# Performance work log

Hardware: AMD Instinct MI355X
Metric: run time of the kernel (lower is better)

The kernel has to match this reference:

```python
import jax, jax.numpy as jnp
import numpy as np

B, S, D, H = 4, 2048, 1024, 16
DK = D // H

def setup_inputs() -> dict:
    key = jax.random.key(0)
    ks = jax.random.split(key, 11)
    sc = 1.0 / np.sqrt(D)
    return {
        "query": jax.random.normal(ks[0], (B, S, D), jnp.float32),
        "key": jax.random.normal(ks[1], (B, S, D), jnp.float32),
        "value": jax.random.normal(ks[2], (B, S, D), jnp.float32),
        "Wq": jax.random.normal(ks[3], (D, D), jnp.float32) * sc,
        "bq": jnp.zeros((D,), jnp.float32),
        "Wk": jax.random.normal(ks[4], (D, D), jnp.float32) * sc,
        "bk": jnp.zeros((D,), jnp.float32),
        "Wv": jax.random.normal(ks[5], (D, D), jnp.float32) * sc,
        "bv": jnp.zeros((D,), jnp.float32),
        "Wo": jax.random.normal(ks[6], (D, D), jnp.float32) * sc,
        "bo": jnp.zeros((D,), jnp.float32),
    }

def _mha(query, key, value, Wq, bq, Wk, bk, Wv, bv, Wo, bo):
    # in_linear{0,1,2}: y = x @ W.T + b  (MetaLinearLayer, weight [out,in])
    def proj(x, W, b):
        y = jnp.einsum('bsd,ed->bse', x, W) + b
        return y.reshape(B, S, H, DK).transpose(0, 2, 1, 3)  # [B,H,S,DK]
    q = proj(query, Wq, bq)
    k = proj(key, Wk, bk)
    v = proj(value, Wv, bv)
    # scores = QK^T / sqrt(d_k)  -> [B,H,S,S] (materialized as in original)
    scores = jnp.einsum('bhqd,bhkd->bhqk', q, k) / jnp.sqrt(jnp.float32(DK))
    p_attn = jax.nn.softmax(scores, axis=-1)
    # dropout is identity in eval/reference mode
    x = jnp.einsum('bhqk,bhkd->bhqd', p_attn, v)
    x = x.transpose(0, 2, 1, 3).reshape(B, S, D)
    return jnp.einsum('bsd,ed->bse', x, Wo) + bo

def reference(query, key, value, Wq, bq, Wk, bk, Wv, bv, Wo, bo):
    return _mha(query, key, value, Wq, bq, Wk, bk, Wv, bv, Wo, bo)
```

## Files before the change

kernel.cpp:

```cpp
#include <hip/hip_runtime.h>
#include <stdint.h>

typedef __attribute__((ext_vector_type(4))) float f32x4;
typedef __attribute__((ext_vector_type(8))) __bf16 bf16x8;
typedef __attribute__((ext_vector_type(8))) unsigned short u16x8;

#define GLOBAL_AS __attribute__((address_space(1)))
#define LDS_AS    __attribute__((address_space(3)))

__device__ __forceinline__ void lds_load16(const void* g, void* l) {
  __builtin_amdgcn_global_load_lds((const GLOBAL_AS uint32_t*)(uintptr_t)g,
                                   (LDS_AS uint32_t*)(uintptr_t)l, 16, 0, 0);
}

__device__ __forceinline__ unsigned short f2bf(float f) {
  uint32_t u = __builtin_bit_cast(uint32_t, f);
  u += 0x7fffu + ((u >> 16) & 1u);
  return (unsigned short)(u >> 16);
}

__device__ __forceinline__ uint32_t pk_bf16(float a, float b) {
#if __has_builtin(__builtin_amdgcn_cvt_pk_bf16_f32)
  return __builtin_bit_cast(uint32_t, __builtin_amdgcn_cvt_pk_bf16_f32(a, b));
#else
  return (uint32_t)f2bf(a) | ((uint32_t)f2bf(b) << 16);
#endif
}

__global__ void cast_all(const float* __restrict__ q, const float* __restrict__ k,
                         const float* __restrict__ v, const float* __restrict__ Wq,
                         const float* __restrict__ Wk, const float* __restrict__ Wv,
                         const float* __restrict__ Wo, unsigned short* __restrict__ dst) {
  const int bid = blockIdx.x;
  const float* src;
  int rel;
  if (bid < 24576) {
    const int seg = bid >> 13;
    rel = bid & 8191;
    src = (seg == 0) ? q : (seg == 1) ? k : v;
  } else {
    const int w = (bid - 24576) >> 10;
    rel = (bid - 24576) & 1023;
    src = (w == 0) ? Wq : (w == 1) ? Wk : (w == 2) ? Wv : Wo;
  }
  const size_t di = (size_t)bid * 1024 + threadIdx.x * 4;
  const size_t si = (size_t)rel * 1024 + threadIdx.x * 4;
  const float4 val = *(const float4*)(src + si);
  ushort4 o;
  o.x = f2bf(val.x); o.y = f2bf(val.y); o.z = f2bf(val.z); o.w = f2bf(val.w);
  *(ushort4*)(dst + di) = o;
}

__global__ __launch_bounds__(256, 2)
void gemm_qkv(const unsigned short* __restrict__ xq, const unsigned short* __restrict__ xk,
              const unsigned short* __restrict__ xv, const unsigned short* __restrict__ wq,
              const unsigned short* __restrict__ wk, const unsigned short* __restrict__ wv,
              const float* __restrict__ bq, const float* __restrict__ bk,
              const float* __restrict__ bv,
              unsigned short* __restrict__ Qh, unsigned short* __restrict__ Kh,
              unsigned short* __restrict__ Vt)
{
  __shared__ __align__(16) unsigned short As[128 * 32];
  __shared__ __align__(16) unsigned short Bs[128 * 32];

  const int gy = blockIdx.y, gx = blockIdx.x;
  const unsigned short* A  = (gy == 0) ? xq : (gy == 1) ? xk : wv;
  const unsigned short* Bw = (gy == 0) ? wq : (gy == 1) ? wk : xv;
  const float* bias        = (gy == 0) ? bq : (gy == 1) ? bk : bv;

  int m0, n0, N;
  if (gy < 2) { m0 = (gx >> 3) * 128; n0 = (gx & 7) * 128; N = 1024; }
  else        { m0 = (gx & 7) * 128;  n0 = (gx >> 3) * 128; N = 8192; }
  const int K = 1024;

  const int tid  = threadIdx.x;
  const int wave = tid >> 6;
  const int lane = tid & 63;
  const int wm = wave >> 1, wn = wave & 1;
  const int quad = lane >> 4, l15 = lane & 15;

  f32x4 acc[4][4];
#pragma unroll
  for (int i = 0; i < 4; ++i)
#pragma unroll
    for (int j = 0; j < 4; ++j) acc[i][j] = f32x4{0.f, 0.f, 0.f, 0.f};

  const int sr = lane >> 2;
  const int sc = (lane & 3) * 8;
  const unsigned short* Ag0 = A  + (size_t)(m0 + wave * 16 + sr) * K + sc;
  const unsigned short* Ag1 = Ag0 + (size_t)64 * K;
  const unsigned short* Bg0 = Bw + (size_t)(n0 + wave * 16 + sr) * K + sc;
  const unsigned short* Bg1 = Bg0 + (size_t)64 * K;
  unsigned short* AsW0 = &As[wave * 512];
  unsigned short* AsW1 = &As[2048 + wave * 512];
  unsigned short* BsW0 = &Bs[wave * 512];
  unsigned short* BsW1 = &Bs[2048 + wave * 512];

  for (int k0 = 0; k0 < K; k0 += 32) {
    lds_load16(Ag0 + k0, AsW0);
    lds_load16(Ag1 + k0, AsW1);
    lds_load16(Bg0 + k0, BsW0);
    lds_load16(Bg1 + k0, BsW1);
    __syncthreads();

    bf16x8 af[4], bfr[4];
#pragma unroll
    for (int i = 0; i < 4; ++i)
      af[i] = *(const bf16x8*)&As[(wm * 64 + i * 16 + l15) * 32 + quad * 8];
#pragma unroll
    for (int j = 0; j < 4; ++j)
      bfr[j] = *(const bf16x8*)&Bs[(wn * 64 + j * 16 + l15) * 32 + quad * 8];
#pragma unroll
    for (int i = 0; i < 4; ++i)
#pragma unroll
      for (int j = 0; j < 4; ++j)
        acc[i][j] = __builtin_amdgcn_mfma_f32_16x16x32_bf16(af[i], bfr[j], acc[i][j], 0, 0, 0);
    __syncthreads();
  }

  if (gy < 2) {
    unsigned short* out = (gy == 0) ? Qh : Kh;
    float bj[4];
#pragma unroll
    for (int j = 0; j < 4; ++j) bj[j] = bias[n0 + wn * 64 + j * 16 + l15];
#pragma unroll
    for (int i = 0; i < 4; ++i) {
      const int mbase = m0 + wm * 64 + i * 16 + quad * 4;
#pragma unroll
      for (int j = 0; j < 4; ++j) {
        const int n = n0 + wn * 64 + j * 16 + l15;
#pragma unroll
        for (int r = 0; r < 4; ++r) {
          const int m = mbase + r;
          const float vv = acc[i][j][r] + bj[j];
          const size_t idx = ((((size_t)(m >> 11) * 16 + (n >> 6)) << 11) + (size_t)(m & 2047)) * 64 + (n & 63);
          out[idx] = f2bf(vv);
        }
      }
    }
  } else {
#pragma unroll
    for (int i = 0; i < 4; ++i) {
      const int mbase = m0 + wm * 64 + i * 16 + quad * 4;
      float bm[4];
#pragma unroll
      for (int r = 0; r < 4; ++r) bm[r] = bias[mbase + r];
#pragma unroll
      for (int j = 0; j < 4; ++j) {
        const int n = n0 + wn * 64 + j * 16 + l15;
#pragma unroll
        for (int r = 0; r < 4; ++r)
          Vt[(size_t)(mbase + r) * N + n] = f2bf(acc[i][j][r] + bm[r]);
      }
    }
  }
}

__global__ __launch_bounds__(256, 2)
void flash_attn(const unsigned short* __restrict__ Qh,
                const unsigned short* __restrict__ Kh,
                const unsigned short* __restrict__ VtG,
                unsigned short* __restrict__ Xo)
{
  __shared__ __align__(16) unsigned short Ks[128 * 72];
  __shared__ __align__(16) unsigned short Vs[64 * 136];
  __shared__ __align__(16) unsigned short Ps[128 * 136];

  const int qb = blockIdx.x, h = blockIdx.y, b = blockIdx.z;
  const int tid = threadIdx.x, wave = tid >> 6, lane = tid & 63;
  const int quad = lane >> 4, l15 = lane & 15;

  const size_t bh = (((size_t)b * 16 + h) << 17);
  const unsigned short* Qg = Qh + bh + ((size_t)qb << 13);
  const unsigned short* Kg = Kh + bh;
  const unsigned short* Vg = VtG + ((size_t)(h * 64)) * 8192 + (size_t)b * 2048;

#pragma unroll
  for (int p = 0; p < 4; ++p) {
    const int c = tid + p * 256;
    u16x8 qv = *(const u16x8*)(Qg + c * 8);
    *(u16x8*)&Ps[(c >> 3) * 136 + (c & 7) * 8] = qv;
  }
  __syncthreads();
  bf16x8 aq[2][2];
#pragma unroll
  for (int i = 0; i < 2; ++i)
#pragma unroll
    for (int d = 0; d < 2; ++d)
      aq[i][d] = *(const bf16x8*)&Ps[(wave * 32 + i * 16 + l15) * 136 + d * 32 + quad * 8];

  f32x4 oacc[2][4];
  float mrow[2], lrow[2];
#pragma unroll
  for (int i = 0; i < 2; ++i) {
#pragma unroll
    for (int jd = 0; jd < 4; ++jd) oacc[i][jd] = f32x4{0.f, 0.f, 0.f, 0.f};
    mrow[i] = -1e30f; lrow[i] = 0.f;
  }

  u16x8 kreg[4], vreg[4];
#pragma unroll
  for (int p = 0; p < 4; ++p) {
    const int c = tid + p * 256;
    kreg[p] = *(const u16x8*)(Kg + c * 8);
    vreg[p] = *(const u16x8*)(Vg + (size_t)(c >> 4) * 8192 + (c & 15) * 8);
  }

  for (int kb = 0; kb < 16; ++kb) {
    __syncthreads();
#pragma unroll
    for (int p = 0; p < 4; ++p) {
      const int c = tid + p * 256;
      *(u16x8*)&Ks[(c >> 3) * 72 + (c & 7) * 8] = kreg[p];
      *(u16x8*)&Vs[(c >> 4) * 136 + (c & 15) * 8] = vreg[p];
    }
    if (kb < 15) {
      const size_t ko = ((size_t)(kb + 1) << 13);
#pragma unroll
      for (int p = 0; p < 4; ++p) {
        const int c = tid + p * 256;
        kreg[p] = *(const u16x8*)(Kg + ko + c * 8);
        vreg[p] = *(const u16x8*)(Vg + (size_t)(c >> 4) * 8192 + (kb + 1) * 128 + (c & 15) * 8);
      }
    }
    __syncthreads();

    f32x4 s[2][8];
#pragma unroll
    for (int i = 0; i < 2; ++i)
#pragma unroll
      for (int j = 0; j < 8; ++j) s[i][j] = f32x4{0.f, 0.f, 0.f, 0.f};
#pragma unroll
    for (int d = 0; d < 2; ++d)
#pragma unroll
      for (int j = 0; j < 8; ++j) {
        bf16x8 kf = *(const bf16x8*)&Ks[(j * 16 + l15) * 72 + d * 32 + quad * 8];
#pragma unroll
        for (int i = 0; i < 2; ++i)
          s[i][j] = __builtin_amdgcn_mfma_f32_16x16x32_bf16(kf, aq[i][d], s[i][j], 0, 0, 0);
      }

#pragma unroll
    for (int i = 0; i < 2; ++i) {
      float mx = -1e30f;
#pragma unroll
      for (int j = 0; j < 8; ++j)
#pragma unroll
        for (int r = 0; r < 4; ++r) {
          s[i][j][r] *= 0.125f;
          mx = fmaxf(mx, s[i][j][r]);
        }
      mx = fmaxf(mx, __shfl_xor(mx, 16));
      mx = fmaxf(mx, __shfl_xor(mx, 32));
      const float mo = mrow[i];
      const float mn = fmaxf(mo, mx);
      mrow[i] = mn;
      const float al = __expf(mo - mn);
      float rs = 0.f;
#pragma unroll
      for (int j = 0; j < 8; ++j)
#pragma unroll
        for (int r = 0; r < 4; ++r) {
          const float p = __expf(s[i][j][r] - mn);
          s[i][j][r] = p;
          rs += p;
        }
      rs += __shfl_xor(rs, 16);
      rs += __shfl_xor(rs, 32);
      lrow[i] = lrow[i] * al + rs;

#pragma unroll
      for (int r = 0; r < 4; ++r) {
        const float aO = __shfl(al, quad * 4 + r);
#pragma unroll
        for (int jd = 0; jd < 4; ++jd) oacc[i][jd][r] *= aO;
      }

      const int prow = (wave * 32 + i * 16 + l15) * 136;
#pragma unroll
      for (int j = 0; j < 8; ++j) {
        uint2 pk;
        pk.x = pk_bf16(s[i][j][0], s[i][j][1]);
        pk.y = pk_bf16(s[i][j][2], s[i][j][3]);
        *(uint2*)&Ps[prow + j * 16 + quad * 4] = pk;
      }
    }

    asm volatile("" ::: "memory");

#pragma unroll
    for (int kk = 0; kk < 4; ++kk) {
      bf16x8 ap[2];
#pragma unroll
      for (int i = 0; i < 2; ++i)
        ap[i] = *(const bf16x8*)&Ps[(wave * 32 + i * 16 + l15) * 136 + kk * 32 + quad * 8];
#pragma unroll
      for (int jd = 0; jd < 4; ++jd) {
        bf16x8 bv = *(const bf16x8*)&Vs[(jd * 16 + l15) * 136 + kk * 32 + quad * 8];
#pragma unroll
        for (int i = 0; i < 2; ++i)
          oacc[i][jd] = __builtin_amdgcn_mfma_f32_16x16x32_bf16(ap[i], bv, oacc[i][jd], 0, 0, 0);
      }
    }
  }

#pragma unroll
  for (int i = 0; i < 2; ++i)
#pragma unroll
    for (int r = 0; r < 4; ++r) {
      const float lO = __shfl(lrow[i], quad * 4 + r);
      const float inv = 1.f / lO;
      const int srow = qb * 128 + wave * 32 + i * 16 + quad * 4 + r;
      const size_t obase = (((size_t)b << 11) + srow) * 1024 + (h << 6);
#pragma unroll
      for (int jd = 0; jd < 4; ++jd)
        Xo[obase + jd * 16 + l15] = f2bf(oacc[i][jd][r] * inv);
    }
}

__global__ __launch_bounds__(256, 2)
void gemm_out(const unsigned short* __restrict__ A,
              const unsigned short* __restrict__ Bw,
              const float* __restrict__ bias,
              float* __restrict__ Cout)
{
  __shared__ __align__(16) unsigned short As[128 * 32];
  __shared__ __align__(16) unsigned short Bs[128 * 32];

  const int tid  = threadIdx.x;
  const int wave = tid >> 6;
  const int lane = tid & 63;
  const int wm = wave >> 1, wn = wave & 1;
  const int quad = lane >> 4, l15 = lane & 15;
  const int m0 = blockIdx.y * 128;
  const int n0 = blockIdx.x * 128;
  const int K = 1024, N = 1024;

  f32x4 acc[4][4];
#pragma unroll
  for (int i = 0; i < 4; ++i)
#pragma unroll
    for (int j = 0; j < 4; ++j) acc[i][j] = f32x4{0.f, 0.f, 0.f, 0.f};

  const int sr = lane >> 2;
  const int sc = (lane & 3) * 8;
  const unsigned short* Ag0 = A  + (size_t)(m0 + wave * 16 + sr) * K + sc;
  const unsigned short* Ag1 = Ag0 + (size_t)64 * K;
  const unsigned short* Bg0 = Bw + (size_t)(n0 + wave * 16 + sr) * K + sc;
  const unsigned short* Bg1 = Bg0 + (size_t)64 * K;
  unsigned short* AsW0 = &As[wave * 512];
  unsigned short* AsW1 = &As[2048 + wave * 512];
  unsigned short* BsW0 = &Bs[wave * 512];
  unsigned short* BsW1 = &Bs[2048 + wave * 512];

  for (int k0 = 0; k0 < K; k0 += 32) {
    lds_load16(Ag0 + k0, AsW0);
    lds_load16(Ag1 + k0, AsW1);
    lds_load16(Bg0 + k0, BsW0);
    lds_load16(Bg1 + k0, BsW1);
    __syncthreads();

    bf16x8 af[4], bfr[4];
#pragma unroll
    for (int i = 0; i < 4; ++i)
      af[i] = *(const bf16x8*)&As[(wm * 64 + i * 16 + l15) * 32 + quad * 8];
#pragma unroll
    for (int j = 0; j < 4; ++j)
      bfr[j] = *(const bf16x8*)&Bs[(wn * 64 + j * 16 + l15) * 32 + quad * 8];
#pragma unroll
    for (int i = 0; i < 4; ++i)
#pragma unroll
      for (int j = 0; j < 4; ++j)
        acc[i][j] = __builtin_amdgcn_mfma_f32_16x16x32_bf16(af[i], bfr[j], acc[i][j], 0, 0, 0);
    __syncthreads();
  }

  float bj[4];
#pragma unroll
  for (int j = 0; j < 4; ++j) bj[j] = bias[n0 + wn * 64 + j * 16 + l15];

#pragma unroll
  for (int i = 0; i < 4; ++i) {
    const int mbase = m0 + wm * 64 + i * 16 + quad * 4;
#pragma unroll
    for (int j = 0; j < 4; ++j) {
      const int n = n0 + wn * 64 + j * 16 + l15;
#pragma unroll
      for (int r = 0; r < 4; ++r)
        Cout[(size_t)(mbase + r) * N + n] = acc[i][j][r] + bj[j];
    }
  }
}

extern "C" void kernel_launch(void* const* d_in, const int* in_sizes, int n_in,
                              void* d_out, int out_size, void* d_ws, size_t ws_size,
                              hipStream_t stream) {
  const float* q  = (const float*)d_in[0];
  const float* k  = (const float*)d_in[1];
  const float* v  = (const float*)d_in[2];
  const float* Wq = (const float*)d_in[3];
  const float* bq = (const float*)d_in[4];
  const float* Wk = (const float*)d_in[5];
  const float* bk = (const float*)d_in[6];
  const float* Wv = (const float*)d_in[7];
  const float* bv = (const float*)d_in[8];
  const float* Wo = (const float*)d_in[9];
  const float* bo = (const float*)d_in[10];

  const int B = 4, S = 2048, D = 1024, H = 16;
  const size_t NX = (size_t)B * S * D;
  const size_t NW = (size_t)D * D;

  unsigned short* xq = (unsigned short*)d_ws;
  unsigned short* xk = xq + NX;
  unsigned short* xv = xk + NX;
  unsigned short* wq = xv + NX;
  unsigned short* wk = wq + NW;
  unsigned short* wv = wk + NW;
  unsigned short* wo = wv + NW;
  unsigned short* Qh = wo + NW;
  unsigned short* Kh = Qh + NX;
  unsigned short* Vt = Kh + NX;
  unsigned short* xo = Vt + NX;

  cast_all<<<28672, 256, 0, stream>>>(q, k, v, Wq, Wk, Wv, Wo, xq);

  gemm_qkv<<<dim3(512, 3), 256, 0, stream>>>(xq, xk, xv, wq, wk, wv, bq, bk, bv, Qh, Kh, Vt);

  flash_attn<<<dim3(S / 128, H, B), 256, 0, stream>>>(Qh, Kh, Vt, xo);

  gemm_out<<<dim3(D / 128, (B * S) / 128), 256, 0, stream>>>(xo, wo, bo, (float*)d_out);
}
```

Measured before the change: 399.6 us.

## Keep softmax probabilities in registers via permuted K rows, drop P LDS buffer

Flash attention now permutes the K rows as they are stored to LDS, so the QK^T MFMA output lanes line up with the A-operand layout the PV MFMA expects. The probabilities are packed straight from registers into bf16 fragments, which removes the P shared-memory buffer and its write/read round trip. With less LDS in use, launch bounds go from 2 to 4 blocks per CU. The softmax also switches to exp2 with log2(e) folded into the scale factor. The risks are extra register pressure under the tighter launch bound and getting the lane permutation wrong.

```diff
diff --git a/kernel.cpp b/kernel.cpp
--- a/kernel.cpp
+++ b/kernel.cpp
@@ -4,6 +4,7 @@
 typedef __attribute__((ext_vector_type(4))) float f32x4;
 typedef __attribute__((ext_vector_type(8))) __bf16 bf16x8;
 typedef __attribute__((ext_vector_type(8))) unsigned short u16x8;
+typedef __attribute__((ext_vector_type(4))) uint32_t u32x4;
 
 #define GLOBAL_AS __attribute__((address_space(1)))
 #define LDS_AS    __attribute__((address_space(3)))
@@ -25,6 +26,23 @@
 #else
   return (uint32_t)f2bf(a) | ((uint32_t)f2bf(b) << 16);
 #endif
+}
+
+__device__ __forceinline__ float exp2f_fast(float x) {
+#if __has_builtin(__builtin_amdgcn_exp2f)
+  return __builtin_amdgcn_exp2f(x);
+#else
+  return __expf(x * 0.6931471805599453f);
+#endif
+}
+
+__device__ __forceinline__ bf16x8 pack8(const f32x4 a, const f32x4 b) {
+  u32x4 d;
+  d.x = pk_bf16(a[0], a[1]);
+  d.y = pk_bf16(a[2], a[3]);
+  d.z = pk_bf16(b[0], b[1]);
+  d.w = pk_bf16(b[2], b[3]);
+  return __builtin_bit_cast(bf16x8, d);
 }
 
 __global__ void cast_all(const float* __restrict__ q, const float* __restrict__ k,
@@ -156,7 +174,7 @@
   }
 }
 
-__global__ __launch_bounds__(256, 2)
+__global__ __launch_bounds__(256, 4)
 void flash_attn(const unsigned short* __restrict__ Qh,
                 const unsigned short* __restrict__ Kh,
                 const unsigned short* __restrict__ VtG,
@@ -164,7 +182,6 @@
 {
   __shared__ __align__(16) unsigned short Ks[128 * 72];
   __shared__ __align__(16) unsigned short Vs[64 * 136];
-  __shared__ __align__(16) unsigned short Ps[128 * 136];
 
   const int qb = blockIdx.x, h = blockIdx.y, b = blockIdx.z;
   const int tid = threadIdx.x, wave = tid >> 6, lane = tid & 63;
@@ -179,7 +196,7 @@
   for (int p = 0; p < 4; ++p) {
     const int c = tid + p * 256;
     u16x8 qv = *(const u16x8*)(Qg + c * 8);
-    *(u16x8*)&Ps[(c >> 3) * 136 + (c & 7) * 8] = qv;
+    *(u16x8*)&Ks[(c >> 3) * 72 + (c & 7) * 8] = qv;
   }
   __syncthreads();
   bf16x8 aq[2][2];
@@ -187,7 +204,7 @@
   for (int i = 0; i < 2; ++i)
 #pragma unroll
     for (int d = 0; d < 2; ++d)
-      aq[i][d] = *(const bf16x8*)&Ps[(wave * 32 + i * 16 + l15) * 136 + d * 32 + quad * 8];
+      aq[i][d] = *(const bf16x8*)&Ks[(wave * 32 + i * 16 + l15) * 72 + d * 32 + quad * 8];
 
   f32x4 oacc[2][4];
   float mrow[2], lrow[2];
@@ -197,6 +214,10 @@
     for (int jd = 0; jd < 4; ++jd) oacc[i][jd] = f32x4{0.f, 0.f, 0.f, 0.f};
     mrow[i] = -1e30f; lrow[i] = 0.f;
   }
+
+  const int rb = (l15 >> 3) * 16 + ((l15 >> 2) & 1) * 4 + (l15 & 3);
+
+  const float SCALE = 0.18033688011112042f;
 
   u16x8 kreg[4], vreg[4];
 #pragma unroll
@@ -211,7 +232,9 @@
 #pragma unroll
     for (int p = 0; p < 4; ++p) {
       const int c = tid + p * 256;
-      *(u16x8*)&Ks[(c >> 3) * 72 + (c & 7) * 8] = kreg[p];
+      const int kr = c >> 3;
+      const int krp = (kr & ~12) | ((kr & 4) << 1) | ((kr & 8) >> 1);
+      *(u16x8*)&Ks[krp * 72 + (c & 7) * 8] = kreg[p];
       *(u16x8*)&Vs[(c >> 4) * 136 + (c & 15) * 8] = vreg[p];
     }
     if (kb < 15) {
@@ -234,7 +257,8 @@
     for (int d = 0; d < 2; ++d)
 #pragma unroll
       for (int j = 0; j < 8; ++j) {
-        bf16x8 kf = *(const bf16x8*)&Ks[(j * 16 + l15) * 72 + d * 32 + quad * 8];
+        const int kk = j >> 1, p2 = j & 1;
+        bf16x8 kf = *(const bf16x8*)&Ks[(kk * 32 + p2 * 8 + rb) * 72 + d * 32 + quad * 8];
 #pragma unroll
         for (int i = 0; i < 2; ++i)
           s[i][j] = __builtin_amdgcn_mfma_f32_16x16x32_bf16(kf, aq[i][d], s[i][j], 0, 0, 0);
@@ -247,7 +271,7 @@
       for (int j = 0; j < 8; ++j)
 #pragma unroll
         for (int r = 0; r < 4; ++r) {
-          s[i][j][r] *= 0.125f;
+          s[i][j][r] *= SCALE;
           mx = fmaxf(mx, s[i][j][r]);
         }
       mx = fmaxf(mx, __shfl_xor(mx, 16));
@@ -255,13 +279,13 @@
       const float mo = mrow[i];
       const float mn = fmaxf(mo, mx);
       mrow[i] = mn;
-      const float al = __expf(mo - mn);
+      const float al = exp2f_fast(mo - mn);
       float rs = 0.f;
 #pragma unroll
       for (int j = 0; j < 8; ++j)
 #pragma unroll
         for (int r = 0; r < 4; ++r) {
-          const float p = __expf(s[i][j][r] - mn);
+          const float p = exp2f_fast(s[i][j][r] - mn);
           s[i][j][r] = p;
           rs += p;
         }
@@ -275,25 +299,14 @@
 #pragma unroll
         for (int jd = 0; jd < 4; ++jd) oacc[i][jd][r] *= aO;
       }
-
-      const int prow = (wave * 32 + i * 16 + l15) * 136;
-#pragma unroll
-      for (int j = 0; j < 8; ++j) {
-        uint2 pk;
-        pk.x = pk_bf16(s[i][j][0], s[i][j][1]);
-        pk.y = pk_bf16(s[i][j][2], s[i][j][3]);
-        *(uint2*)&Ps[prow + j * 16 + quad * 4] = pk;
-      }
-    }
-
-    asm volatile("" ::: "memory");
+    }
 
 #pragma unroll
     for (int kk = 0; kk < 4; ++kk) {
       bf16x8 ap[2];
 #pragma unroll
       for (int i = 0; i < 2; ++i)
-        ap[i] = *(const bf16x8*)&Ps[(wave * 32 + i * 16 + l15) * 136 + kk * 32 + quad * 8];
+        ap[i] = pack8(s[i][2 * kk], s[i][2 * kk + 1]);
 #pragma unroll
       for (int jd = 0; jd < 4; ++jd) {
         bf16x8 bv = *(const bf16x8*)&Vs[(jd * 16 + l15) * 136 + kk * 32 + quad * 8];
@@ -424,10 +437,7 @@
   unsigned short* xo = Vt + NX;
 
   cast_all<<<28672, 256, 0, stream>>>(q, k, v, Wq, Wk, Wv, Wo, xq);
-
   gemm_qkv<<<dim3(512, 3), 256, 0, stream>>>(xq, xk, xv, wq, wk, wv, bq, bk, bv, Qh, Kh, Vt);
-
   flash_attn<<<dim3(S / 128, H, B), 256, 0, stream>>>(Qh, Kh, Vt, xo);
-
   gemm_out<<<dim3(D / 128, (B * S) / 128), 256, 0, stream>>>(xo, wo, bo, (float*)d_out);
 }
```

Measured after the change: 634.8 us. 1.59x slower.
